# Kernel tuning notes

Measured on AMD Instinct MI355X. Metric: run time of the kernel, lower is better.

Reference implementation:

```python
import jax, jax.numpy as jnp
import numpy as np

B, N, IN_F = 4, 2048, 256
H, HEAD_DIM = 8, 32  # out_features=256, concat=True -> head_dim=32
ALPHA = 0.2
MASK_VAL = -9e15


def setup_inputs() -> dict:
    key = jax.random.key(0)
    k1, k2, k3, k4 = jax.random.split(key, 4)
    x = jax.random.normal(k1, (B, N, IN_F), dtype=jnp.float32)
    adj = jax.random.randint(k2, (B, N, N), 0, 2, dtype=jnp.int32)
    # xavier_uniform for W [H, in, head_dim]: gain=1, fan_in=in, fan_out=head_dim
    limW = float(np.sqrt(6.0 / (IN_F + HEAD_DIM)))
    W = jax.random.uniform(k3, (H, IN_F, HEAD_DIM), dtype=jnp.float32, minval=-limW, maxval=limW)
    # xavier_uniform for a [H, 2*head_dim]: fan_in=2*head_dim, fan_out=H (2D tensor)
    lima = float(np.sqrt(6.0 / (H + 2 * HEAD_DIM)))
    a = jax.random.uniform(k4, (H, 2 * HEAD_DIM), dtype=jnp.float32, minval=-lima, maxval=lima)
    return {"x": x, "adj": adj, "W": W, "a": a}


def reference(x, adj, W, a):
    # x: [B, N, F], adj: [B, N, N], W: [H, F, D], a: [H, 2D]
    D = W.shape[-1]
    Wh = jnp.einsum('bnf,hfd->bhnd', x, W)                     # [B,H,N,D]
    a_src, a_dst = a[:, :D], a[:, D:]
    # additive score e_ij = a_src . Wh_i + a_dst . Wh_j (equivalent to concat+matmul)
    e_i = jnp.einsum('bhnd,hd->bhn', Wh, a_src)                # [B,H,N]
    e_j = jnp.einsum('bhnd,hd->bhn', Wh, a_dst)                # [B,H,N]
    scores = e_i[:, :, :, None] + e_j[:, :, None, :]           # [B,H,N,N]
    scores = jnp.where(scores > 0, scores, ALPHA * scores)     # LeakyReLU
    scores = jnp.where(adj[:, None, :, :] == 0, MASK_VAL, scores)
    probs = jax.nn.softmax(scores, axis=-1)                    # [B,H,N,N]
    h = jnp.einsum('bhij,bhjd->bhid', probs, Wh)               # [B,H,N,D]
    b, n = x.shape[0], x.shape[1]
    return h.transpose(0, 2, 1, 3).reshape(b, n, h.shape[1] * D)  # concat heads
```

## Files before the change

### kernel.cpp

```cpp
#include <hip/hip_runtime.h>

#define BB 4
#define NN 2048
#define INF 256
#define HH 8
#define DD 32
#define LOG2E 1.4426950408889634f

typedef __attribute__((ext_vector_type(8))) short short8;
typedef __attribute__((ext_vector_type(4))) float f32x4;

__device__ __forceinline__ unsigned short bf16_rne(float v) {
    unsigned b = __float_as_uint(v);
    return (unsigned short)((b + 0x7fffu + ((b >> 16) & 1u)) >> 16);
}
__device__ __forceinline__ unsigned short bf16_rhu(float v) {
    return (unsigned short)((__float_as_uint(v) + 0x8000u) >> 16);
}

__global__ __launch_bounds__(256) void wprep_kernel(
    const float* __restrict__ W, const float* __restrict__ a,
    float* __restrict__ we_g, unsigned short* __restrict__ wT)
{
    const int bb = blockIdx.x, t = threadIdx.x;
    if (bb < 16) {
        const int h = bb & 7, sel = bb >> 3;
        const float* wr = W + ((size_t)(h * INF + t)) * DD;
        const float* av = a + h * 2 * DD + sel * DD;
        float acc = 0.f;
        #pragma unroll
        for (int d = 0; d < DD; ++d) acc += wr[d] * av[d];
        we_g[bb * INF + t] = acc * LOG2E;
    }
    #pragma unroll
    for (int r2 = 0; r2 < 8; ++r2) {
        int row = bb * 8 + r2;
        int h = row >> 5, d = row & 31;
        wT[row * INF + t] = bf16_rhu(W[((size_t)(h * INF + t)) * DD + d]);
    }
}

__global__ __launch_bounds__(256) void ek_kernel(
    const float* __restrict__ x, const float* __restrict__ we_g,
    float* __restrict__ esrc, unsigned* __restrict__ ejP)
{
    __shared__ __align__(16) float xs[16 * 260];
    __shared__ __align__(16) float weld2[16 * 260];
    const int t = threadIdx.x;
    const int tile = blockIdx.x & 127, b = blockIdx.x >> 7;
    const int n0 = tile * 16;

    #pragma unroll
    for (int p = 0; p < 4; ++p) {
        int flat = p * 1024 + t * 4;
        int row = flat >> 8, col = flat & 255;
        f32x4 g = *(const f32x4*)&x[((size_t)(b * NN + n0 + row)) * INF + col];
        *(f32x4*)&xs[row * 260 + col] = g;
    }
    #pragma unroll
    for (int p = 0; p < 4; ++p) {
        int flat = p * 1024 + t * 4;
        int k = flat >> 8, f = flat & 255;
        f32x4 g = *(const f32x4*)&we_g[flat];
        *(f32x4*)&weld2[(f >> 4) * 260 + k * 16 + (f & 15)] = g;
    }
    __syncthreads();

    const int row = t >> 4, c = t & 15;
    f32x4 xv[4];
    #pragma unroll
    for (int i = 0; i < 4; ++i)
        xv[i] = *(const f32x4*)&xs[row * 260 + c * 16 + i * 4];

    float keep = 0.f;
    #pragma unroll
    for (int k = 0; k < 16; ++k) {
        float s = 0.f;
        #pragma unroll
        for (int i = 0; i < 4; ++i) {
            f32x4 w4 = *(const f32x4*)&weld2[c * 260 + k * 16 + i * 4];
            s += xv[i][0]*w4[0] + xv[i][1]*w4[1] + xv[i][2]*w4[2] + xv[i][3]*w4[3];
        }
        s += __shfl_xor(s, 1, 64);
        s += __shfl_xor(s, 2, 64);
        s += __shfl_xor(s, 4, 64);
        s += __shfl_xor(s, 8, 64);
        keep = (c == k) ? s : keep;
    }
    const int n = n0 + row;
    if (c < 8) {
        esrc[(b * 8 + c) * NN + n] = keep;
    } else {
        float Ej  = __builtin_amdgcn_exp2f(keep);
        float Ej5 = __builtin_amdgcn_exp2f(0.2f * keep);
        ejP[(b * 8 + (c - 8)) * NN + n] =
            ((unsigned)bf16_rne(Ej) << 16) | (unsigned)bf16_rne(Ej5);
    }
}

__global__ __launch_bounds__(256) void whk_kernel(
    const float* __restrict__ x, const unsigned short* __restrict__ wT,
    unsigned short* __restrict__ whT2)
{
    __shared__ __align__(16) unsigned short xb[64 * 264];
    __shared__ __align__(16) unsigned short wb[64 * 264];
    const int t = threadIdx.x;
    const int hp = blockIdx.x & 3, tl = (blockIdx.x >> 2) & 31, b = blockIdx.x >> 7;
    const int n0 = tl * 64;

    #pragma unroll
    for (int p = 0; p < 16; ++p) {
        int flat = p * 1024 + t * 4;
        int row = flat >> 8, col = flat & 255;
        f32x4 g = *(const f32x4*)&x[((size_t)(b * NN + n0 + row)) * INF + col];
        unsigned a0 = __float_as_uint(g[0]) + 0x8000u;
        unsigned a1 = __float_as_uint(g[1]) + 0x8000u;
        unsigned a2 = __float_as_uint(g[2]) + 0x8000u;
        unsigned a3 = __float_as_uint(g[3]) + 0x8000u;
        uint2 pk;
        pk.x = __builtin_amdgcn_perm(a1, a0, 0x07060302u);
        pk.y = __builtin_amdgcn_perm(a3, a2, 0x07060302u);
        *(uint2*)&xb[row * 264 + col] = pk;
    }
    #pragma unroll
    for (int p = 0; p < 8; ++p) {
        int flat = p * 2048 + t * 8;
        int cc = flat >> 8, f = flat & 255;
        *(short8*)&wb[cc * 264 + f] = *(const short8*)&wT[(hp * 64 + cc) * INF + f];
    }
    __syncthreads();

    const int w = t >> 6, l = t & 63;
    const int ml = l & 15, q = l >> 4;
    f32x4 acc[4] = {};
    const unsigned short* ap = &xb[(w * 16 + ml) * 264 + q * 8];
    #pragma unroll
    for (int k0 = 0; k0 < INF; k0 += 32) {
        short8 A = *(const short8*)&ap[k0];
        #pragma unroll
        for (int c16 = 0; c16 < 4; ++c16) {
            short8 Bf = *(const short8*)&wb[(c16 * 16 + ml) * 264 + q * 8 + k0];
            acc[c16] = __builtin_amdgcn_mfma_f32_16x16x32_bf16(A, Bf, acc[c16], 0, 0, 0);
        }
    }
    __syncthreads();

    unsigned short* ldsC = xb;
    #pragma unroll
    for (int c16 = 0; c16 < 4; ++c16)
        #pragma unroll
        for (int r = 0; r < 4; ++r) {
            int col = c16 * 16 + ml;
            int rt  = w * 16 + q * 4 + r;
            ldsC[col * 72 + rt] = bf16_rhu(acc[c16][r]);
        }
    __syncthreads();

    #pragma unroll
    for (int p = 0; p < 2; ++p) {
        int g = p * 256 + t;
        int d = g & 31, jo = (g >> 5) & 7, h2 = g >> 8;
        short8 vv = *(const short8*)&ldsC[(h2 * 32 + d) * 72 + jo * 8];
        int bh = b * 8 + hp * 2 + h2;
        *(short8*)&whT2[(((size_t)bh * 256 + tl * 8 + jo) * 32 + d) * 8] = vv;
    }
}

__global__ __launch_bounds__(1024, 4) void attn_kernel(
    const int* __restrict__ adj, const unsigned short* __restrict__ whT2,
    const float* __restrict__ esrc, const unsigned* __restrict__ ejP,
    float* __restrict__ out)
{
    __shared__ __align__(16) unsigned bits[2][2][32][4];
    __shared__ __align__(16) float cmb[8][64][25];
    const int t = threadIdx.x, v = t >> 6, l = t & 63;
    const int h = v & 7, js = v >> 3;
    const int ml = l & 15, q = l >> 4;
    const int it = blockIdx.x & 63, b = blockIdx.x >> 6;
    const int i0 = it * 32;
    const int bh = b * HH + h;

    const float ei0 = esrc[bh * NN + i0 + ml];
    const float ei1 = esrc[bh * NN + i0 + 16 + ml];
    const float Ei0  = __builtin_amdgcn_exp2f(ei0);
    const float Ei05 = __builtin_amdgcn_exp2f(0.2f * ei0);
    const float Ei1  = __builtin_amdgcn_exp2f(ei1);
    const float Ei15 = __builtin_amdgcn_exp2f(0.2f * ei1);

    const unsigned* epP = ejP + bh * NN + js * 1024;
    const unsigned short* whb = whT2 + ((size_t)bh * 256 + js * 128) * 256;

    const int* gbase[4];
    #pragma unroll
    for (int u = 0; u < 4; ++u) {
        int uid = v * 4 + u;
        int row = uid & 31, half = uid >> 5;
        gbase[u] = adj + ((size_t)(b * NN + i0 + row)) * NN + half * 1024 + l;
    }

    auto stage_load = [&](int c2, int* ra, int* rb) {
        #pragma unroll
        for (int u = 0; u < 4; ++u) {
            const int* g = gbase[u] + c2 * 128;
            ra[u] = g[0];
            rb[u] = g[64];
        }
    };
    auto stage_commit = [&](const int* ra, const int* rb, int buf) {
        #pragma unroll
        for (int u = 0; u < 4; ++u) {
            int uid = v * 4 + u;
            int row = uid & 31, half = uid >> 5;
            unsigned long long m0 = __ballot(ra[u] != 0);
            unsigned long long m1 = __ballot(rb[u] != 0);
            if (l == 0) {
                uint4 pv = make_uint4((unsigned)m0, (unsigned)(m0 >> 32),
                                      (unsigned)m1, (unsigned)(m1 >> 32));
                *(uint4*)&bits[buf][half][row][0] = pv;
            }
        }
    };

    const short8 ones = {0x3F80, 0x3F80, 0x3F80, 0x3F80, 0x3F80, 0x3F80, 0x3F80, 0x3F80};
    f32x4 acc00 = {}, acc01 = {}, acc10 = {}, acc11 = {}, accD0 = {}, accD1 = {};

    int rA0[4], rA1[4], rB0[4], rB1[4];
    stage_load(0, rA0, rA1);
    stage_load(1, rB0, rB1);
    stage_commit(rA0, rA1, 0);

    for (int c = 0; c < 8; ++c) {
        __syncthreads();
        if (c < 7) {
            if (c & 1) stage_commit(rA0, rA1, (c + 1) & 1);
            else       stage_commit(rB0, rB1, (c + 1) & 1);
        }
        if (c < 6) {
            if (c & 1) stage_load(c + 2, rB0, rB1);
            else       stage_load(c + 2, rA0, rA1);
        }
        const int buf = c & 1;
        unsigned w0a[4], w1a[4];
        *(uint4*)w0a = *(const uint4*)&bits[buf][js][ml][0];
        *(uint4*)w1a = *(const uint4*)&bits[buf][js][16 + ml][0];
        const unsigned* epc = epP + c * 128;
        #pragma unroll
        for (int k = 0; k < 4; ++k) {
            const int jb = k * 32 + q * 8;
            uint4 epA = *(const uint4*)&epc[jb];
            uint4 epB = *(const uint4*)&epc[jb + 4];
            const unsigned short* wp = whb + (size_t)(c * 16 + k * 4 + q) * 256;
            short8 B0 = *(const short8*)&wp[ml * 8];
            short8 B1 = *(const short8*)&wp[(16 + ml) * 8];
            unsigned st0 = w0a[k] >> (q * 8);
            unsigned st1 = w1a[k] >> (q * 8);
            union { unsigned u[4]; short8 s; } f0, f1;
            const unsigned* ea = &epA.x;
            const unsigned* eb = &epB.x;
            #pragma unroll
            for (int pp = 0; pp < 4; ++pp) {
                unsigned pkA = (pp < 2) ? ea[2 * pp]     : eb[2 * pp - 4];
                unsigned pkB = (pp < 2) ? ea[2 * pp + 1] : eb[2 * pp - 3];
                float EjA = __uint_as_float(pkA & 0xffff0000u);
                float FjA = __uint_as_float(pkA << 16);
                float EjB = __uint_as_float(pkB & 0xffff0000u);
                float FjB = __uint_as_float(pkB << 16);
                unsigned mA0 = (unsigned)__builtin_amdgcn_sbfe(st0, 2 * pp, 1);
                unsigned mB0 = (unsigned)__builtin_amdgcn_sbfe(st0, 2 * pp + 1, 1);
                unsigned mA1 = (unsigned)__builtin_amdgcn_sbfe(st1, 2 * pp, 1);
                unsigned mB1 = (unsigned)__builtin_amdgcn_sbfe(st1, 2 * pp + 1, 1);
                float pA0 = fmaxf(EjA * Ei0, FjA * Ei05);
                float pB0 = fmaxf(EjB * Ei0, FjB * Ei05);
                float pA1 = fmaxf(EjA * Ei1, FjA * Ei15);
                float pB1 = fmaxf(EjB * Ei1, FjB * Ei15);
                f0.u[pp] = __builtin_amdgcn_perm(__float_as_uint(pB0) & mB0,
                                                 __float_as_uint(pA0) & mA0,
                                                 0x07060302u);
                f1.u[pp] = __builtin_amdgcn_perm(__float_as_uint(pB1) & mB1,
                                                 __float_as_uint(pA1) & mA1,
                                                 0x07060302u);
            }
            acc00 = __builtin_amdgcn_mfma_f32_16x16x32_bf16(f0.s, B0, acc00, 0, 0, 0);
            acc01 = __builtin_amdgcn_mfma_f32_16x16x32_bf16(f0.s, B1, acc01, 0, 0, 0);
            accD0 = __builtin_amdgcn_mfma_f32_16x16x32_bf16(f0.s, ones, accD0, 0, 0, 0);
            acc10 = __builtin_amdgcn_mfma_f32_16x16x32_bf16(f1.s, B0, acc10, 0, 0, 0);
            acc11 = __builtin_amdgcn_mfma_f32_16x16x32_bf16(f1.s, B1, acc11, 0, 0, 0);
            accD1 = __builtin_amdgcn_mfma_f32_16x16x32_bf16(f1.s, ones, accD1, 0, 0, 0);
        }
    }

    float* myc = &cmb[h][l][0];
    if (js == 1) {
        *(f32x4*)&myc[0]  = acc00; *(f32x4*)&myc[4]  = acc01;
        *(f32x4*)&myc[8]  = acc10; *(f32x4*)&myc[12] = acc11;
        *(f32x4*)&myc[16] = accD0; *(f32x4*)&myc[20] = accD1;
    }
    __syncthreads();
    if (js == 0) {
        f32x4 o00 = *(const f32x4*)&myc[0],  o01 = *(const f32x4*)&myc[4];
        f32x4 o10 = *(const f32x4*)&myc[8],  o11 = *(const f32x4*)&myc[12];
        f32x4 oD0 = *(const f32x4*)&myc[16], oD1 = *(const f32x4*)&myc[20];
        #pragma unroll
        for (int r = 0; r < 4; ++r) {
            int ir0 = i0 + q * 4 + r;
            int ir1 = i0 + 16 + q * 4 + r;
            float inv0 = 1.0f / (accD0[r] + oD0[r]);
            float inv1 = 1.0f / (accD1[r] + oD1[r]);
            size_t ba0 = ((size_t)(b * NN + ir0)) * (HH * DD) + h * DD;
            size_t ba1 = ((size_t)(b * NN + ir1)) * (HH * DD) + h * DD;
            out[ba0 + ml]      = (acc00[r] + o00[r]) * inv0;
            out[ba0 + 16 + ml] = (acc01[r] + o01[r]) * inv0;
            out[ba1 + ml]      = (acc10[r] + o10[r]) * inv1;
            out[ba1 + 16 + ml] = (acc11[r] + o11[r]) * inv1;
        }
    }
}

extern "C" void kernel_launch(void* const* d_in, const int* in_sizes, int n_in,
                              void* d_out, int out_size, void* d_ws, size_t ws_size,
                              hipStream_t stream) {
    (void)in_sizes; (void)n_in; (void)out_size; (void)ws_size;
    const float* x   = (const float*)d_in[0];
    const int*   adj = (const int*)d_in[1];
    const float* W   = (const float*)d_in[2];
    const float* a   = (const float*)d_in[3];
    float* out = (float*)d_out;

    char* ws = (char*)d_ws;
    unsigned short* whT2 = (unsigned short*)ws;
    unsigned short* wT   = (unsigned short*)(ws + (4u << 20));
    float*    esrc = (float*)(ws + (4u << 20) + (128u << 10));
    unsigned* ejP  = (unsigned*)(esrc + BB * HH * NN);
    float*    we_g = (float*)(ejP + BB * HH * NN);

    wprep_kernel<<<dim3(32),  dim3(256), 0, stream>>>(W, a, we_g, wT);
    ek_kernel  <<<dim3(512),  dim3(256), 0, stream>>>(x, we_g, esrc, ejP);
    whk_kernel <<<dim3(512),  dim3(256), 0, stream>>>(x, wT, whT2);
    attn_kernel<<<dim3(256),  dim3(1024), 0, stream>>>(adj, whT2, esrc, ejP, out);
}
```

Measured before the change: 150.2 us.

## Merge prep kernels into one role-split launch and precompute adjacency bitmask

```diff
diff --git a/kernel.cpp b/kernel.cpp
--- a/kernel.cpp
+++ b/kernel.cpp
@@ -18,36 +18,108 @@
     return (unsigned short)((__float_as_uint(v) + 0x8000u) >> 16);
 }
 
-__global__ __launch_bounds__(256) void wprep_kernel(
+__global__ __launch_bounds__(256) void prep_kernel(
+    const float* __restrict__ x, const int* __restrict__ adj,
     const float* __restrict__ W, const float* __restrict__ a,
-    float* __restrict__ we_g, unsigned short* __restrict__ wT)
+    unsigned short* __restrict__ whT2, float* __restrict__ esrc,
+    unsigned* __restrict__ ejP, unsigned* __restrict__ bitsG)
 {
-    const int bb = blockIdx.x, t = threadIdx.x;
-    if (bb < 16) {
-        const int h = bb & 7, sel = bb >> 3;
-        const float* wr = W + ((size_t)(h * INF + t)) * DD;
-        const float* av = a + h * 2 * DD + sel * DD;
-        float acc = 0.f;
-        #pragma unroll
-        for (int d = 0; d < DD; ++d) acc += wr[d] * av[d];
-        we_g[bb * INF + t] = acc * LOG2E;
-    }
-    #pragma unroll
-    for (int r2 = 0; r2 < 8; ++r2) {
-        int row = bb * 8 + r2;
-        int h = row >> 5, d = row & 31;
-        wT[row * INF + t] = bf16_rhu(W[((size_t)(h * INF + t)) * DD + d]);
-    }
-}
-
-__global__ __launch_bounds__(256) void ek_kernel(
-    const float* __restrict__ x, const float* __restrict__ we_g,
-    float* __restrict__ esrc, unsigned* __restrict__ ejP)
-{
-    __shared__ __align__(16) float xs[16 * 260];
-    __shared__ __align__(16) float weld2[16 * 260];
-    const int t = threadIdx.x;
-    const int tile = blockIdx.x & 127, b = blockIdx.x >> 7;
+    __shared__ __align__(16) unsigned short smem[64 * 264 * 2];
+    const int bid = blockIdx.x, t = threadIdx.x;
+    const int role = bid & 3;
+
+    if (role >= 2) {
+        const int id = (bid >> 2) * 2 + (role - 2);
+        const int w64 = t & 63;
+        #pragma unroll
+        for (int rr = 0; rr < 2; ++rr) {
+            int row = id * 8 + (t >> 6) + rr * 4;
+            const int* ap = adj + (size_t)row * NN + w64 * 32;
+            unsigned word = 0;
+            #pragma unroll
+            for (int u = 0; u < 8; ++u) {
+                int4 g = *(const int4*)&ap[u * 4];
+                unsigned nib = (g.x != 0 ? 1u : 0u) | (g.y != 0 ? 2u : 0u)
+                             | (g.z != 0 ? 4u : 0u) | (g.w != 0 ? 8u : 0u);
+                word |= nib << (u * 4);
+            }
+            bitsG[(size_t)row * 64 + w64] = word;
+        }
+        return;
+    }
+
+    if (role == 0) {
+        unsigned short* xb = smem;
+        unsigned short* wb = smem + 64 * 264;
+        const int id = bid >> 2;
+        const int hp = id & 3, tl = (id >> 2) & 31, b = id >> 7;
+        const int n0 = tl * 64;
+
+        #pragma unroll
+        for (int p = 0; p < 16; ++p) {
+            int flat = p * 1024 + t * 4;
+            int row = flat >> 8, col = flat & 255;
+            f32x4 g = *(const f32x4*)&x[((size_t)(b * NN + n0 + row)) * INF + col];
+            unsigned a0 = __float_as_uint(g[0]) + 0x8000u;
+            unsigned a1 = __float_as_uint(g[1]) + 0x8000u;
+            unsigned a2 = __float_as_uint(g[2]) + 0x8000u;
+            unsigned a3 = __float_as_uint(g[3]) + 0x8000u;
+            uint2 pk;
+            pk.x = __builtin_amdgcn_perm(a1, a0, 0x07060302u);
+            pk.y = __builtin_amdgcn_perm(a3, a2, 0x07060302u);
+            *(uint2*)&xb[row * 264 + col] = pk;
+        }
+        #pragma unroll
+        for (int p = 0; p < 16; ++p) {
+            int flat = p * 1024 + t * 4;
+            int h2 = flat >> 13, rem = flat & 8191;
+            int f = rem >> 5, d0 = rem & 31;
+            f32x4 g = *(const f32x4*)&W[(((size_t)(hp * 2 + h2)) * INF + f) * DD + d0];
+            #pragma unroll
+            for (int i = 0; i < 4; ++i)
+                wb[(h2 * 32 + d0 + i) * 264 + f] = bf16_rhu(g[i]);
+        }
+        __syncthreads();
+
+        const int w = t >> 6, l = t & 63;
+        const int ml = l & 15, q = l >> 4;
+        f32x4 acc[4] = {};
+        const unsigned short* apx = &xb[(w * 16 + ml) * 264 + q * 8];
+        #pragma unroll
+        for (int k0 = 0; k0 < INF; k0 += 32) {
+            short8 A = *(const short8*)&apx[k0];
+            #pragma unroll
+            for (int c16 = 0; c16 < 4; ++c16) {
+                short8 Bf = *(const short8*)&wb[(c16 * 16 + ml) * 264 + q * 8 + k0];
+                acc[c16] = __builtin_amdgcn_mfma_f32_16x16x32_bf16(A, Bf, acc[c16], 0, 0, 0);
+            }
+        }
+        __syncthreads();
+        unsigned short* ldsC = xb;
+        #pragma unroll
+        for (int c16 = 0; c16 < 4; ++c16)
+            #pragma unroll
+            for (int r = 0; r < 4; ++r) {
+                int col = c16 * 16 + ml;
+                int rt  = w * 16 + q * 4 + r;
+                ldsC[col * 72 + rt] = bf16_rhu(acc[c16][r]);
+            }
+        __syncthreads();
+        #pragma unroll
+        for (int p = 0; p < 2; ++p) {
+            int g = p * 256 + t;
+            int d = g & 31, jo = (g >> 5) & 7, h2 = g >> 8;
+            short8 vv = *(const short8*)&ldsC[(h2 * 32 + d) * 72 + jo * 8];
+            int bh = b * 8 + hp * 2 + h2;
+            *(short8*)&whT2[(((size_t)bh * 256 + tl * 8 + jo) * 32 + d) * 8] = vv;
+        }
+        return;
+    }
+
+    float* xs    = (float*)smem;
+    float* weld2 = (float*)smem + 16 * 260;
+    const int id = bid >> 2;
+    const int tile = id & 127, b = id >> 7;
     const int n0 = tile * 16;
 
     #pragma unroll
@@ -57,20 +129,29 @@
         f32x4 g = *(const f32x4*)&x[((size_t)(b * NN + n0 + row)) * INF + col];
         *(f32x4*)&xs[row * 260 + col] = g;
     }
-    #pragma unroll
-    for (int p = 0; p < 4; ++p) {
-        int flat = p * 1024 + t * 4;
-        int k = flat >> 8, f = flat & 255;
-        f32x4 g = *(const f32x4*)&we_g[flat];
-        *(f32x4*)&weld2[(f >> 4) * 260 + k * 16 + (f & 15)] = g;
+    {
+        const int f = t;
+        #pragma unroll
+        for (int h = 0; h < 8; ++h) {
+            const float* wr = W + ((size_t)(h * INF + f)) * DD;
+            float s0 = 0.f, s1 = 0.f;
+            #pragma unroll
+            for (int d = 0; d < DD; ++d) {
+                float wv = wr[d];
+                s0 += wv * a[h * 2 * DD + d];
+                s1 += wv * a[h * 2 * DD + DD + d];
+            }
+            weld2[(f >> 4) * 260 + h * 16 + (f & 15)]       = s0 * LOG2E;
+            weld2[(f >> 4) * 260 + (h + 8) * 16 + (f & 15)] = s1 * LOG2E;
+        }
     }
     __syncthreads();
 
-    const int row = t >> 4, c = t & 15;
+    const int row = t >> 4, cc = t & 15;
     f32x4 xv[4];
     #pragma unroll
     for (int i = 0; i < 4; ++i)
-        xv[i] = *(const f32x4*)&xs[row * 260 + c * 16 + i * 4];
+        xv[i] = *(const f32x4*)&xs[row * 260 + cc * 16 + i * 4];
 
     float keep = 0.f;
     #pragma unroll
@@ -78,183 +159,66 @@
         float s = 0.f;
         #pragma unroll
         for (int i = 0; i < 4; ++i) {
-            f32x4 w4 = *(const f32x4*)&weld2[c * 260 + k * 16 + i * 4];
+            f32x4 w4 = *(const f32x4*)&weld2[cc * 260 + k * 16 + i * 4];
             s += xv[i][0]*w4[0] + xv[i][1]*w4[1] + xv[i][2]*w4[2] + xv[i][3]*w4[3];
         }
         s += __shfl_xor(s, 1, 64);
         s += __shfl_xor(s, 2, 64);
         s += __shfl_xor(s, 4, 64);
         s += __shfl_xor(s, 8, 64);
-        keep = (c == k) ? s : keep;
+        keep = (cc == k) ? s : keep;
     }
     const int n = n0 + row;
-    if (c < 8) {
-        esrc[(b * 8 + c) * NN + n] = keep;
+    if (cc < 8) {
+        esrc[(b * 8 + cc) * NN + n] = keep;
     } else {
         float Ej  = __builtin_amdgcn_exp2f(keep);
         float Ej5 = __builtin_amdgcn_exp2f(0.2f * keep);
-        ejP[(b * 8 + (c - 8)) * NN + n] =
+        ejP[(b * 8 + (cc - 8)) * NN + n] =
             ((unsigned)bf16_rne(Ej) << 16) | (unsigned)bf16_rne(Ej5);
     }
 }
 
-__global__ __launch_bounds__(256) void whk_kernel(
-    const float* __restrict__ x, const unsigned short* __restrict__ wT,
-    unsigned short* __restrict__ whT2)
-{
-    __shared__ __align__(16) unsigned short xb[64 * 264];
-    __shared__ __align__(16) unsigned short wb[64 * 264];
-    const int t = threadIdx.x;
-    const int hp = blockIdx.x & 3, tl = (blockIdx.x >> 2) & 31, b = blockIdx.x >> 7;
-    const int n0 = tl * 64;
-
-    #pragma unroll
-    for (int p = 0; p < 16; ++p) {
-        int flat = p * 1024 + t * 4;
-        int row = flat >> 8, col = flat & 255;
-        f32x4 g = *(const f32x4*)&x[((size_t)(b * NN + n0 + row)) * INF + col];
-        unsigned a0 = __float_as_uint(g[0]) + 0x8000u;
-        unsigned a1 = __float_as_uint(g[1]) + 0x8000u;
-        unsigned a2 = __float_as_uint(g[2]) + 0x8000u;
-        unsigned a3 = __float_as_uint(g[3]) + 0x8000u;
-        uint2 pk;
-        pk.x = __builtin_amdgcn_perm(a1, a0, 0x07060302u);
-        pk.y = __builtin_amdgcn_perm(a3, a2, 0x07060302u);
-        *(uint2*)&xb[row * 264 + col] = pk;
-    }
-    #pragma unroll
-    for (int p = 0; p < 8; ++p) {
-        int flat = p * 2048 + t * 8;
-        int cc = flat >> 8, f = flat & 255;
-        *(short8*)&wb[cc * 264 + f] = *(const short8*)&wT[(hp * 64 + cc) * INF + f];
-    }
-    __syncthreads();
-
-    const int w = t >> 6, l = t & 63;
-    const int ml = l & 15, q = l >> 4;
-    f32x4 acc[4] = {};
-    const unsigned short* ap = &xb[(w * 16 + ml) * 264 + q * 8];
-    #pragma unroll
-    for (int k0 = 0; k0 < INF; k0 += 32) {
-        short8 A = *(const short8*)&ap[k0];
-        #pragma unroll
-        for (int c16 = 0; c16 < 4; ++c16) {
-            short8 Bf = *(const short8*)&wb[(c16 * 16 + ml) * 264 + q * 8 + k0];
-            acc[c16] = __builtin_amdgcn_mfma_f32_16x16x32_bf16(A, Bf, acc[c16], 0, 0, 0);
-        }
-    }
-    __syncthreads();
-
-    unsigned short* ldsC = xb;
-    #pragma unroll
-    for (int c16 = 0; c16 < 4; ++c16)
-        #pragma unroll
-        for (int r = 0; r < 4; ++r) {
-            int col = c16 * 16 + ml;
-            int rt  = w * 16 + q * 4 + r;
-            ldsC[col * 72 + rt] = bf16_rhu(acc[c16][r]);
-        }
-    __syncthreads();
-
-    #pragma unroll
-    for (int p = 0; p < 2; ++p) {
-        int g = p * 256 + t;
-        int d = g & 31, jo = (g >> 5) & 7, h2 = g >> 8;
-        short8 vv = *(const short8*)&ldsC[(h2 * 32 + d) * 72 + jo * 8];
-        int bh = b * 8 + hp * 2 + h2;
-        *(short8*)&whT2[(((size_t)bh * 256 + tl * 8 + jo) * 32 + d) * 8] = vv;
-    }
-}
-
-__global__ __launch_bounds__(1024, 4) void attn_kernel(
-    const int* __restrict__ adj, const unsigned short* __restrict__ whT2,
-    const float* __restrict__ esrc, const unsigned* __restrict__ ejP,
+__global__ __launch_bounds__(256, 4) void attn_kernel(
+    const unsigned short* __restrict__ whT2, const float* __restrict__ esrc,
+    const unsigned* __restrict__ ejP, const unsigned* __restrict__ bitsG,
     float* __restrict__ out)
 {
-    __shared__ __align__(16) unsigned bits[2][2][32][4];
-    __shared__ __align__(16) float cmb[8][64][25];
     const int t = threadIdx.x, v = t >> 6, l = t & 63;
-    const int h = v & 7, js = v >> 3;
     const int ml = l & 15, q = l >> 4;
-    const int it = blockIdx.x & 63, b = blockIdx.x >> 6;
-    const int i0 = it * 32;
+    const int bid = blockIdx.x;
+    const int hg = bid & 1;
+    const int it = (bid >> 1) & 127;
+    const int b = bid >> 8;
+    const int h = hg * 4 + v;
+    const int i0 = it * 16;
     const int bh = b * HH + h;
 
-    const float ei0 = esrc[bh * NN + i0 + ml];
-    const float ei1 = esrc[bh * NN + i0 + 16 + ml];
-    const float Ei0  = __builtin_amdgcn_exp2f(ei0);
-    const float Ei05 = __builtin_amdgcn_exp2f(0.2f * ei0);
-    const float Ei1  = __builtin_amdgcn_exp2f(ei1);
-    const float Ei15 = __builtin_amdgcn_exp2f(0.2f * ei1);
-
-    const unsigned* epP = ejP + bh * NN + js * 1024;
-    const unsigned short* whb = whT2 + ((size_t)bh * 256 + js * 128) * 256;
-
-    const int* gbase[4];
-    #pragma unroll
-    for (int u = 0; u < 4; ++u) {
-        int uid = v * 4 + u;
-        int row = uid & 31, half = uid >> 5;
-        gbase[u] = adj + ((size_t)(b * NN + i0 + row)) * NN + half * 1024 + l;
-    }
-
-    auto stage_load = [&](int c2, int* ra, int* rb) {
-        #pragma unroll
-        for (int u = 0; u < 4; ++u) {
-            const int* g = gbase[u] + c2 * 128;
-            ra[u] = g[0];
-            rb[u] = g[64];
-        }
-    };
-    auto stage_commit = [&](const int* ra, const int* rb, int buf) {
-        #pragma unroll
-        for (int u = 0; u < 4; ++u) {
-            int uid = v * 4 + u;
-            int row = uid & 31, half = uid >> 5;
-            unsigned long long m0 = __ballot(ra[u] != 0);
-            unsigned long long m1 = __ballot(rb[u] != 0);
-            if (l == 0) {
-                uint4 pv = make_uint4((unsigned)m0, (unsigned)(m0 >> 32),
-                                      (unsigned)m1, (unsigned)(m1 >> 32));
-                *(uint4*)&bits[buf][half][row][0] = pv;
-            }
-        }
-    };
-
-    const short8 ones = {0x3F80, 0x3F80, 0x3F80, 0x3F80, 0x3F80, 0x3F80, 0x3F80, 0x3F80};
-    f32x4 acc00 = {}, acc01 = {}, acc10 = {}, acc11 = {}, accD0 = {}, accD1 = {};
-
-    int rA0[4], rA1[4], rB0[4], rB1[4];
-    stage_load(0, rA0, rA1);
-    stage_load(1, rB0, rB1);
-    stage_commit(rA0, rA1, 0);
-
-    for (int c = 0; c < 8; ++c) {
-        __syncthreads();
-        if (c < 7) {
-            if (c & 1) stage_commit(rA0, rA1, (c + 1) & 1);
-            else       stage_commit(rB0, rB1, (c + 1) & 1);
-        }
-        if (c < 6) {
-            if (c & 1) stage_load(c + 2, rB0, rB1);
-            else       stage_load(c + 2, rA0, rA1);
-        }
-        const int buf = c & 1;
-        unsigned w0a[4], w1a[4];
-        *(uint4*)w0a = *(const uint4*)&bits[buf][js][ml][0];
-        *(uint4*)w1a = *(const uint4*)&bits[buf][js][16 + ml][0];
+    const float ei = esrc[bh * NN + i0 + ml];
+    const float Gi = __builtin_amdgcn_exp2f(-0.8f * ei);
+
+    const unsigned* epP = ejP + bh * NN;
+    const unsigned short* whb = whT2 + (size_t)bh * (256 * DD * 8);
+    const unsigned* mbase = bitsG + ((size_t)(b * NN + i0 + ml)) * 64;
+
+    const short8 ones = {0x3F80, 0x3F80, 0x3F80, 0x3F80,
+                         0x3F80, 0x3F80, 0x3F80, 0x3F80};
+    f32x4 accP = {}, accQ = {}, accD = {};
+
+    for (int c = 0; c < 16; ++c) {
+        uint4 mrow = *(const uint4*)&mbase[c * 4];
         const unsigned* epc = epP + c * 128;
+        const unsigned mw[4] = {mrow.x, mrow.y, mrow.z, mrow.w};
         #pragma unroll
         for (int k = 0; k < 4; ++k) {
             const int jb = k * 32 + q * 8;
             uint4 epA = *(const uint4*)&epc[jb];
             uint4 epB = *(const uint4*)&epc[jb + 4];
-            const unsigned short* wp = whb + (size_t)(c * 16 + k * 4 + q) * 256;
+            const unsigned short* wp = whb + (size_t)((c * 16 + k * 4 + q) * 256);
             short8 B0 = *(const short8*)&wp[ml * 8];
             short8 B1 = *(const short8*)&wp[(16 + ml) * 8];
-            unsigned st0 = w0a[k] >> (q * 8);
-            unsigned st1 = w1a[k] >> (q * 8);
-            union { unsigned u[4]; short8 s; } f0, f1;
+            unsigned st = mw[k] >> (q * 8);
+            union { unsigned u[4]; short8 s; } f0;
             const unsigned* ea = &epA.x;
             const unsigned* eb = &epB.x;
             #pragma unroll
@@ -265,54 +229,27 @@
                 float FjA = __uint_as_float(pkA << 16);
                 float EjB = __uint_as_float(pkB & 0xffff0000u);
                 float FjB = __uint_as_float(pkB << 16);
-                unsigned mA0 = (unsigned)__builtin_amdgcn_sbfe(st0, 2 * pp, 1);
-                unsigned mB0 = (unsigned)__builtin_amdgcn_sbfe(st0, 2 * pp + 1, 1);
-                unsigned mA1 = (unsigned)__builtin_amdgcn_sbfe(st1, 2 * pp, 1);
-                unsigned mB1 = (unsigned)__builtin_amdgcn_sbfe(st1, 2 * pp + 1, 1);
-                float pA0 = fmaxf(EjA * Ei0, FjA * Ei05);
-                float pB0 = fmaxf(EjB * Ei0, FjB * Ei05);
-                float pA1 = fmaxf(EjA * Ei1, FjA * Ei15);
-                float pB1 = fmaxf(EjB * Ei1, FjB * Ei15);
-                f0.u[pp] = __builtin_amdgcn_perm(__float_as_uint(pB0) & mB0,
-                                                 __float_as_uint(pA0) & mA0,
+                unsigned mA = (unsigned)__builtin_amdgcn_sbfe(st, 2 * pp, 1);
+                unsigned mB = (unsigned)__builtin_amdgcn_sbfe(st, 2 * pp + 1, 1);
+                float pA = fmaxf(EjA, FjA * Gi);
+                float pB = fmaxf(EjB, FjB * Gi);
+                f0.u[pp] = __builtin_amdgcn_perm(__float_as_uint(pB) & mB,
+                                                 __float_as_uint(pA) & mA,
                                                  0x07060302u);
-                f1.u[pp] = __builtin_amdgcn_perm(__float_as_uint(pB1) & mB1,
-                                                 __float_as_uint(pA1) & mA1,
-                                                 0x07060302u);
-            }
-            acc00 = __builtin_amdgcn_mfma_f32_16x16x32_bf16(f0.s, B0, acc00, 0, 0, 0);
-            acc01 = __builtin_amdgcn_mfma_f32_16x16x32_bf16(f0.s, B1, acc01, 0, 0, 0);
-            accD0 = __builtin_amdgcn_mfma_f32_16x16x32_bf16(f0.s, ones, accD0, 0, 0, 0);
-            acc10 = __builtin_amdgcn_mfma_f32_16x16x32_bf16(f1.s, B0, acc10, 0, 0, 0);
-            acc11 = __builtin_amdgcn_mfma_f32_16x16x32_bf16(f1.s, B1, acc11, 0, 0, 0);
-            accD1 = __builtin_amdgcn_mfma_f32_16x16x32_bf16(f1.s, ones, accD1, 0, 0, 0);
-        }
-    }
-
-    float* myc = &cmb[h][l][0];
-    if (js == 1) {
-        *(f32x4*)&myc[0]  = acc00; *(f32x4*)&myc[4]  = acc01;
-        *(f32x4*)&myc[8]  = acc10; *(f32x4*)&myc[12] = acc11;
-        *(f32x4*)&myc[16] = accD0; *(f32x4*)&myc[20] = accD1;
-    }
-    __syncthreads();
-    if (js == 0) {
-        f32x4 o00 = *(const f32x4*)&myc[0],  o01 = *(const f32x4*)&myc[4];
-        f32x4 o10 = *(const f32x4*)&myc[8],  o11 = *(const f32x4*)&myc[12];
-        f32x4 oD0 = *(const f32x4*)&myc[16], oD1 = *(const f32x4*)&myc[20];
-        #pragma unroll
-        for (int r = 0; r < 4; ++r) {
-            int ir0 = i0 + q * 4 + r;
-            int ir1 = i0 + 16 + q * 4 + r;
-            float inv0 = 1.0f / (accD0[r] + oD0[r]);
-            float inv1 = 1.0f / (accD1[r] + oD1[r]);
-            size_t ba0 = ((size_t)(b * NN + ir0)) * (HH * DD) + h * DD;
-            size_t ba1 = ((size_t)(b * NN + ir1)) * (HH * DD) + h * DD;
-            out[ba0 + ml]      = (acc00[r] + o00[r]) * inv0;
-            out[ba0 + 16 + ml] = (acc01[r] + o01[r]) * inv0;
-            out[ba1 + ml]      = (acc10[r] + o10[r]) * inv1;
-            out[ba1 + 16 + ml] = (acc11[r] + o11[r]) * inv1;
-        }
+            }
+            accP = __builtin_amdgcn_mfma_f32_16x16x32_bf16(f0.s, B0, accP, 0, 0, 0);
+            accQ = __builtin_amdgcn_mfma_f32_16x16x32_bf16(f0.s, B1, accQ, 0, 0, 0);
+            accD = __builtin_amdgcn_mfma_f32_16x16x32_bf16(f0.s, ones, accD, 0, 0, 0);
+        }
+    }
+
+    #pragma unroll
+    for (int r = 0; r < 4; ++r) {
+        int ir = i0 + q * 4 + r;
+        float inv = 1.0f / accD[r];
+        size_t ba = ((size_t)(b * NN + ir)) * (HH * DD) + h * DD;
+        out[ba + ml]      = accP[r] * inv;
+        out[ba + 16 + ml] = accQ[r] * inv;
     }
 }
 
@@ -328,13 +265,11 @@
 
     char* ws = (char*)d_ws;
     unsigned short* whT2 = (unsigned short*)ws;
-    unsigned short* wT   = (unsigned short*)(ws + (4u << 20));
-    float*    esrc = (float*)(ws + (4u << 20) + (128u << 10));
-    unsigned* ejP  = (unsigned*)(esrc + BB * HH * NN);
-    float*    we_g = (float*)(ejP + BB * HH * NN);
-
-    wprep_kernel<<<dim3(32),  dim3(256), 0, stream>>>(W, a, we_g, wT);
-    ek_kernel  <<<dim3(512),  dim3(256), 0, stream>>>(x, we_g, esrc, ejP);
-    whk_kernel <<<dim3(512),  dim3(256), 0, stream>>>(x, wT, whT2);
-    attn_kernel<<<dim3(256),  dim3(1024), 0, stream>>>(adj, whT2, esrc, ejP, out);
-}
+    float*    esrc  = (float*)(ws + (4u << 20));
+    unsigned* ejP   = (unsigned*)(ws + (4u << 20) + (256u << 10));
+    unsigned* bitsG = (unsigned*)(ws + (4u << 20) + (512u << 10));
+
+    prep_kernel<<<dim3(2048), dim3(256), 0, stream>>>(x, adj, W, a,
+                                                      whT2, esrc, ejP, bitsG);
+    attn_kernel<<<dim3(1024), dim3(256), 0, stream>>>(whT2, esrc, ejP, bitsG, out);
+}
```

Measured after the change: 197.1 us. 31.2% more time.
